# Optimization experiments

Hardware: AMD Instinct MI355X
Metric: run time of the kernel (lower is better)

## Reference

```python
import jax, jax.numpy as jnp
import numpy as np

T, B = 64, 64
E, H, V, L = 512, 1024, 32000, 2


def setup_inputs() -> dict:
    key = jax.random.key(0)
    ks = jax.random.split(key, 16)
    s = 0.05  # weight scale for numerical sanity
    return {
        "dec_input": jax.random.randint(ks[0], (T, B), 0, V),
        "enc_outputs": jax.random.normal(ks[1], (B, 48, H), jnp.float32),
        "h0": jax.random.normal(ks[2], (L, B, H), jnp.float32),
        "c0": jax.random.normal(ks[3], (L, B, H), jnp.float32),
        "emb_W": jax.random.normal(ks[4], (V, E), jnp.float32) * s,
        "W_ih0": jax.random.normal(ks[5], (4 * H, E), jnp.float32) * s,
        "W_hh0": jax.random.normal(ks[6], (4 * H, H), jnp.float32) * s,
        "b_ih0": jax.random.normal(ks[7], (4 * H,), jnp.float32) * s,
        "b_hh0": jax.random.normal(ks[8], (4 * H,), jnp.float32) * s,
        "W_ih1": jax.random.normal(ks[9], (4 * H, H), jnp.float32) * s,
        "W_hh1": jax.random.normal(ks[10], (4 * H, H), jnp.float32) * s,
        "b_ih1": jax.random.normal(ks[11], (4 * H,), jnp.float32) * s,
        "b_hh1": jax.random.normal(ks[12], (4 * H,), jnp.float32) * s,
        "W_out": jax.random.normal(ks[13], (V, H), jnp.float32) * s,
        "b_out": jax.random.normal(ks[14], (V,), jnp.float32) * s,
    }


def _lstm_cell(x, h, c, Wih, Whh, bih, bhh):
    # PyTorch LSTMCell gate order: i, f, g, o
    g = x @ Wih.T + bih + h @ Whh.T + bhh  # [B, 4H]
    i, f, gg, o = jnp.split(g, 4, axis=-1)
    c_n = jax.nn.sigmoid(f) * c + jax.nn.sigmoid(i) * jnp.tanh(gg)
    h_n = jax.nn.sigmoid(o) * jnp.tanh(c_n)
    return h_n, c_n


def reference(dec_input, enc_outputs, h0, c0, emb_W,
              W_ih0, W_hh0, b_ih0, b_hh0,
              W_ih1, W_hh1, b_ih1, b_hh1,
              W_out, b_out):
    emb = emb_W[dec_input]            # [T, B, E]
    xs = emb[:-1]                     # inputs for steps 0..T-2
    tgt = dec_input[1:]               # gather targets dec_input[t+1]

    def step(carry, inp):
        h, c, loss = carry            # h,c: [L, B, H]
        x, t = inp
        h0n, c0n = _lstm_cell(x, h[0], c[0], W_ih0, W_hh0, b_ih0, b_hh0)
        h1n, c1n = _lstm_cell(h0n, h[1], c[1], W_ih1, W_hh1, b_ih1, b_hh1)
        logits = h1n @ W_out.T + b_out              # [B, V]
        lp = jax.nn.log_softmax(logits, axis=-1)
        loss = loss - jnp.take_along_axis(lp, t[:, None], axis=1).sum()
        return (jnp.stack([h0n, h1n]), jnp.stack([c0n, c1n]), loss), None

    init = (h0, c0, jnp.zeros((), h0.dtype))
    (_, _, loss), _ = jax.lax.scan(step, init, (xs, tgt))
    return loss
```

## Files before the change

kernel.cpp:

```cpp
#include <hip/hip_runtime.h>
#include <math.h>

#define TSTEPS 63
#define BB 64
#define ED 512
#define HD 1024
#define VV 32000
#define GG 4096
#define NROWS 4032
#define MPAD 4096
#define NCH 500
#define PSTRIDE 262144

typedef __attribute__((ext_vector_type(8))) short short8;
typedef __attribute__((ext_vector_type(4))) float f32x4;

__device__ __forceinline__ float sigf(float x) { return 1.0f / (1.0f + __expf(-x)); }

__device__ __forceinline__ short f2bf(float f) {
  unsigned u = __float_as_uint(f);
  unsigned r = (u + 0x7FFFu + ((u >> 16) & 1u)) >> 16;
  return (short)r;
}

__global__ __launch_bounds__(256)
void init_state_k(const float* __restrict__ h0, const float* __restrict__ c0,
                  float* __restrict__ hs, float* __restrict__ cs) {
  int i = blockIdx.x * 256 + threadIdx.x;
  hs[i] = h0[i];
  cs[i] = c0[i];
}

__global__ __launch_bounds__(256)
void cvt_f2b_k(const float* __restrict__ src, short* __restrict__ dst) {
  int i = (blockIdx.x * 256 + threadIdx.x) * 4;
  float4 v = *(const float4*)(src + i);
  short4 o;
  o.x = f2bf(v.x); o.y = f2bf(v.y); o.z = f2bf(v.z); o.w = f2bf(v.w);
  *(short4*)(dst + i) = o;
}

__global__ __launch_bounds__(256)
void gather_emb_k(const int* __restrict__ dec, const float* __restrict__ emb,
                  short* __restrict__ XembB) {
  int idx = blockIdx.x * 256 + threadIdx.x;
  int r = idx >> 7, cc = (idx & 127) * 4;
  int src = dec[r];
  float4 v = *(const float4*)(emb + (size_t)src * ED + cc);
  short4 o;
  o.x = f2bf(v.x); o.y = f2bf(v.y); o.z = f2bf(v.z); o.w = f2bf(v.w);
  *(short4*)(XembB + (size_t)r * ED + cc) = o;
}

__global__ __launch_bounds__(256)
void pad_h1b_k(short* __restrict__ H1b) {
  int i = (blockIdx.x * 256 + threadIdx.x) * 4;
  short4 z; z.x = z.y = z.z = z.w = 0;
  *(short4*)(H1b + (size_t)NROWS * HD + i) = z;
}

__global__ void zero_out_k(float* __restrict__ out) {
  if (threadIdx.x == 0) out[0] = 0.f;
}

template<int NK>
__device__ __forceinline__ void mfma_loop(const short* __restrict__ Abase, int lda,
                                          const short* __restrict__ Bbase, int ldb,
                                          short* lds_a, short* lds_b,
                                          f32x4 acc[4][4]) {
  const int tid = threadIdx.x;
  const int l = tid & 63;
  const int w = tid >> 6;
  const int wm = w >> 1, wn = w & 1;
  const int p = tid & 7;
  const int rbase = tid >> 3;

  for (int kt = 0; kt < NK; kt++) {
#pragma unroll
    for (int it = 0; it < 4; it++) {
      int row = it * 32 + rbase;
      int ch = p ^ (row & 7);
      const short* ga = Abase + (size_t)row * lda + kt * 64 + ch * 8;
      const short* gb = Bbase + (size_t)row * ldb + kt * 64 + ch * 8;
      short* la = lds_a + it * 2048 + tid * 8;
      short* lb = lds_b + it * 2048 + tid * 8;
      __builtin_amdgcn_global_load_lds((const __attribute__((address_space(1))) void*)ga,
                                       (__attribute__((address_space(3))) void*)la, 16, 0, 0);
      __builtin_amdgcn_global_load_lds((const __attribute__((address_space(1))) void*)gb,
                                       (__attribute__((address_space(3))) void*)lb, 16, 0, 0);
    }
    asm volatile("s_waitcnt vmcnt(0)" ::: "memory");
    __syncthreads();

    short8 af[4][2], bf[4][2];
#pragma unroll
    for (int m = 0; m < 4; m++) {
#pragma unroll
      for (int ks = 0; ks < 2; ks++) {
        int ra = wm * 64 + m * 16 + (l & 15);
        int ca = (ks * 4 + (l >> 4)) ^ (ra & 7);
        af[m][ks] = *(const short8*)(lds_a + ra * 64 + ca * 8);
        int rb = wn * 64 + m * 16 + (l & 15);
        int cb = (ks * 4 + (l >> 4)) ^ (rb & 7);
        bf[m][ks] = *(const short8*)(lds_b + rb * 64 + cb * 8);
      }
    }
#pragma unroll
    for (int ks = 0; ks < 2; ks++)
#pragma unroll
      for (int m = 0; m < 4; m++)
#pragma unroll
        for (int n = 0; n < 4; n++)
          acc[m][n] = __builtin_amdgcn_mfma_f32_16x16x32_bf16(af[m][ks], bf[n][ks],
                                                              acc[m][n], 0, 0, 0);
    __syncthreads();
  }
}

__global__ __launch_bounds__(256)
void x0_mfma_k(const short* __restrict__ XembB, const short* __restrict__ Wih0B,
               const float* __restrict__ bih0, const float* __restrict__ bhh0,
               float* __restrict__ X0) {
  __shared__ short lds_a[128 * 64];
  __shared__ short lds_b[128 * 64];
  f32x4 acc[4][4];
#pragma unroll
  for (int m = 0; m < 4; m++)
#pragma unroll
    for (int n = 0; n < 4; n++)
#pragma unroll
      for (int q = 0; q < 4; q++) acc[m][n][q] = 0.f;

  mfma_loop<8>(XembB + (size_t)blockIdx.x * 128 * ED, ED,
               Wih0B + (size_t)blockIdx.y * 128 * ED, ED, lds_a, lds_b, acc);

  const int l = threadIdx.x & 63;
  const int w = threadIdx.x >> 6;
  const int wm = w >> 1, wn = w & 1;
#pragma unroll
  for (int m = 0; m < 4; m++)
#pragma unroll
    for (int r = 0; r < 4; r++) {
      int row = blockIdx.x * 128 + wm * 64 + m * 16 + (l >> 4) * 4 + r;
#pragma unroll
      for (int n = 0; n < 4; n++) {
        int col = blockIdx.y * 128 + wn * 64 + n * 16 + (l & 15);
        X0[(size_t)row * GG + col] = acc[m][n][r] + bih0[col] + bhh0[col];
      }
    }
}

__global__ __launch_bounds__(256)
void lse_mfma_k(const short* __restrict__ H1b, const short* __restrict__ WoutB,
                const float* __restrict__ bout, float* __restrict__ m_part,
                float* __restrict__ s_part) {
  __shared__ short lds_a[128 * 64];
  __shared__ short lds_b[128 * 64];
  f32x4 acc[4][4];
#pragma unroll
  for (int m = 0; m < 4; m++)
#pragma unroll
    for (int n = 0; n < 4; n++)
#pragma unroll
      for (int q = 0; q < 4; q++) acc[m][n][q] = 0.f;

  mfma_loop<16>(H1b + (size_t)blockIdx.x * 128 * HD, HD,
                WoutB + (size_t)blockIdx.y * 128 * HD, HD, lds_a, lds_b, acc);

  const int l = threadIdx.x & 63;
  const int w = threadIdx.x >> 6;
  const int wm = w >> 1, wn = w & 1;
  const int colbase = blockIdx.y * 128 + wn * 64 + (l & 15);
  float bo[4];
#pragma unroll
  for (int n = 0; n < 4; n++) bo[n] = bout[colbase + n * 16];
  const int ch = blockIdx.y * 2 + wn;

#pragma unroll
  for (int m = 0; m < 4; m++) {
#pragma unroll
    for (int r = 0; r < 4; r++) {
      float v0 = acc[m][0][r] + bo[0];
      float v1 = acc[m][1][r] + bo[1];
      float v2 = acc[m][2][r] + bo[2];
      float v3 = acc[m][3][r] + bo[3];
      float mx = fmaxf(fmaxf(v0, v1), fmaxf(v2, v3));
      float s = __expf(v0 - mx) + __expf(v1 - mx) + __expf(v2 - mx) + __expf(v3 - mx);
#pragma unroll
      for (int off = 1; off < 16; off <<= 1) {
        float mo = __shfl_xor(mx, off);
        float so = __shfl_xor(s, off);
        float nm = fmaxf(mx, mo);
        s = s * __expf(mx - nm) + so * __expf(mo - nm);
        mx = nm;
      }
      if ((l & 15) == 0) {
        int row = blockIdx.x * 128 + wm * 64 + m * 16 + (l >> 4) * 4 + r;
        m_part[(size_t)ch * MPAD + row] = mx;
        s_part[(size_t)ch * MPAD + row] = s;
      }
    }
  }
}

__global__ __launch_bounds__(256)
void rec_gemm_k(const float* __restrict__ A0, const float* __restrict__ W0,
                const float* __restrict__ A1, const float* __restrict__ W1,
                float* __restrict__ part) {
  __shared__ float As[16][68];
  __shared__ float Bs[16][68];
  int n0 = blockIdx.x * 64;
  int p  = blockIdx.y;
  const float* A = (p < 4) ? A0 : A1;
  const float* W = (p < 4) ? W0 : W1;
  int koff = (p & 3) * 256;
  int tid = threadIdx.x;
  int tx = tid & 15, ty = tid >> 4;
  int lm = tid >> 2, lk = (tid & 3) * 4;
  float acc[4][4] = {};
  for (int k0 = koff; k0 < koff + 256; k0 += 16) {
    float4 av = *(const float4*)(A + (size_t)lm * HD + k0 + lk);
    float4 bv = *(const float4*)(W + (size_t)(n0 + lm) * HD + k0 + lk);
    As[lk + 0][lm] = av.x; As[lk + 1][lm] = av.y; As[lk + 2][lm] = av.z; As[lk + 3][lm] = av.w;
    Bs[lk + 0][lm] = bv.x; Bs[lk + 1][lm] = bv.y; Bs[lk + 2][lm] = bv.z; Bs[lk + 3][lm] = bv.w;
    __syncthreads();
#pragma unroll
    for (int kk = 0; kk < 16; kk++) {
      float a4[4], b4[4];
      *(float4*)a4 = *(const float4*)&As[kk][ty * 4];
      *(float4*)b4 = *(const float4*)&Bs[kk][tx * 4];
#pragma unroll
      for (int i = 0; i < 4; i++)
#pragma unroll
        for (int j = 0; j < 4; j++) acc[i][j] += a4[i] * b4[j];
    }
    __syncthreads();
  }
  float* dst = part + (size_t)p * PSTRIDE;
#pragma unroll
  for (int i = 0; i < 4; i++)
#pragma unroll
    for (int j = 0; j < 4; j++)
      dst[(size_t)(ty * 4 + i) * GG + n0 + tx * 4 + j] = acc[i][j];
}

__global__ __launch_bounds__(256)
void cell0_k(const float* __restrict__ X0t, const float* __restrict__ part,
             float* __restrict__ h, float* __restrict__ c) {
  int idx = blockIdx.x * 256 + threadIdx.x;
  int b = idx >> 10, j = idx & (HD - 1);
  float g[4];
#pragma unroll
  for (int q = 0; q < 4; q++) {
    size_t o = (size_t)b * GG + q * HD + j;
    g[q] = X0t[o] + part[o] + part[o + PSTRIDE] + part[o + 2 * PSTRIDE] + part[o + 3 * PSTRIDE];
  }
  float cn = sigf(g[1]) * c[idx] + sigf(g[0]) * tanhf(g[2]);
  float hn = sigf(g[3]) * tanhf(cn);
  c[idx] = cn;
  h[idx] = hn;
}

__global__ __launch_bounds__(256)
void cell1_k(const float* __restrict__ part, const float* __restrict__ bih,
             const float* __restrict__ bhh, float* __restrict__ h,
             float* __restrict__ c, float* __restrict__ H1t,
             short* __restrict__ H1bt) {
  int idx = blockIdx.x * 256 + threadIdx.x;
  int b = idx >> 10, j = idx & (HD - 1);
  float g[4];
#pragma unroll
  for (int q = 0; q < 4; q++) {
    int gi = q * HD + j;
    size_t o = (size_t)b * GG + gi;
    float v = bih[gi] + bhh[gi];
#pragma unroll
    for (int p = 0; p < 8; p++) v += part[(size_t)p * PSTRIDE + o];
    g[q] = v;
  }
  float cn = sigf(g[1]) * c[idx] + sigf(g[0]) * tanhf(g[2]);
  float hn = sigf(g[3]) * tanhf(cn);
  c[idx] = cn;
  h[idx] = hn;
  H1t[idx] = hn;
  H1bt[idx] = f2bf(hn);
}

__global__ __launch_bounds__(256)
void tgt_logit_k(const float* __restrict__ H1, const float* __restrict__ Wout,
                 const float* __restrict__ bout, const int* __restrict__ dec,
                 float* __restrict__ tl) {
  int gw = (blockIdx.x * 256 + threadIdx.x) >> 6;
  int lane = threadIdx.x & 63;
  if (gw >= NROWS) return;
  int tgt = dec[gw + 64];
  const float* hrow = H1 + (size_t)gw * HD;
  const float* wrow = Wout + (size_t)tgt * HD;
  float s = 0.f;
#pragma unroll
  for (int q = 0; q < 16; q++) {
    int k = lane + q * 64;
    s += hrow[k] * wrow[k];
  }
#pragma unroll
  for (int off = 32; off > 0; off >>= 1) s += __shfl_down(s, off);
  if (lane == 0) tl[gw] = s + bout[tgt];
}

__global__ __launch_bounds__(256)
void row_lse_k(const float* __restrict__ m_part, const float* __restrict__ s_part,
               const float* __restrict__ tl, float* __restrict__ out) {
  int row = blockIdx.x * 256 + threadIdx.x;
  float loss = 0.f;
  if (row < NROWS) {
    float M = -INFINITY, S = 0.f;
    for (int ch = 0; ch < NCH; ch++) {
      float m = m_part[(size_t)ch * MPAD + row];
      float s = s_part[(size_t)ch * MPAD + row];
      float nm = fmaxf(M, m);
      S = S * __expf(M - nm) + s * __expf(m - nm);
      M = nm;
    }
    loss = M + logf(S) - tl[row];
  }
  __shared__ float red[256];
  red[threadIdx.x] = loss;
  __syncthreads();
  for (int s = 128; s > 0; s >>= 1) {
    if (threadIdx.x < s) red[threadIdx.x] += red[threadIdx.x + s];
    __syncthreads();
  }
  if (threadIdx.x == 0) atomicAdd(out, red[0]);
}

extern "C" void kernel_launch(void* const* d_in, const int* in_sizes, int n_in,
                              void* d_out, int out_size, void* d_ws, size_t ws_size,
                              hipStream_t stream) {
  const int*   dec  = (const int*)  d_in[0];
  const float* h0   = (const float*)d_in[2];
  const float* c0   = (const float*)d_in[3];
  const float* emb  = (const float*)d_in[4];
  const float* Wih0 = (const float*)d_in[5];
  const float* Whh0 = (const float*)d_in[6];
  const float* bih0 = (const float*)d_in[7];
  const float* bhh0 = (const float*)d_in[8];
  const float* Wih1 = (const float*)d_in[9];
  const float* Whh1 = (const float*)d_in[10];
  const float* bih1 = (const float*)d_in[11];
  const float* bhh1 = (const float*)d_in[12];
  const float* Wout = (const float*)d_in[13];
  const float* bout = (const float*)d_in[14];
  float* out = (float*)d_out;

  float* ws = (float*)d_ws;
  float* X0     = ws;
  float* H1     = X0 + (size_t)MPAD * GG;
  float* hs     = H1 + (size_t)NROWS * HD;
  float* cs     = hs + 2 * BB * HD;
  float* part   = cs + 2 * BB * HD;
  float* m_part = part + 8 * (size_t)BB * GG;
  float* s_part = m_part + (size_t)NCH * MPAD;
  float* tl     = s_part + (size_t)NCH * MPAD;
  short* H1b    = (short*)(tl + MPAD);
  short* WoutB  = H1b + (size_t)MPAD * HD;
  short* Wih0B  = WoutB + (size_t)VV * HD;
  short* XembB  = Wih0B + (size_t)GG * ED;

  float* hs0 = hs, * hs1 = hs + BB * HD;
  float* cs0 = cs, * cs1 = cs + BB * HD;

  init_state_k<<<(2 * BB * HD) / 256, 256, 0, stream>>>(h0, c0, hs, cs);
  cvt_f2b_k<<<(VV * HD) / 1024, 256, 0, stream>>>(Wout, WoutB);
  cvt_f2b_k<<<(GG * ED) / 1024, 256, 0, stream>>>(Wih0, Wih0B);
  gather_emb_k<<<(MPAD * ED / 4) / 256, 256, 0, stream>>>(dec, emb, XembB);
  pad_h1b_k<<<64, 256, 0, stream>>>(H1b);
  zero_out_k<<<1, 64, 0, stream>>>(out);
  x0_mfma_k<<<dim3(MPAD / 128, GG / 128), 256, 0, stream>>>(XembB, Wih0B, bih0, bhh0, X0);

  for (int t = 0; t < TSTEPS; t++) {
    rec_gemm_k<<<dim3(64, 4), 256, 0, stream>>>(hs0, Whh0, hs0, Whh0, part);
    cell0_k<<<256, 256, 0, stream>>>(X0 + (size_t)t * BB * GG, part, hs0, cs0);
    rec_gemm_k<<<dim3(64, 8), 256, 0, stream>>>(hs0, Wih1, hs1, Whh1, part);
    cell1_k<<<256, 256, 0, stream>>>(part, bih1, bhh1, hs1, cs1,
                                     H1 + (size_t)t * BB * HD, H1b + (size_t)t * BB * HD);
  }

  tgt_logit_k<<<(NROWS * 64 + 255) / 256, 256, 0, stream>>>(H1, Wout, bout, dec, tl);
  lse_mfma_k<<<dim3(MPAD / 128, VV / 128), 256, 0, stream>>>(H1b, WoutB, bout, m_part, s_part);
  row_lse_k<<<MPAD / 256, 256, 0, stream>>>(m_part, s_part, tl, out);
}
```

Baseline: 3.319 ms.

## Fuse LSTM recurrence into one persistent cooperative kernel with bf16 MFMA

Replaces the 252 per-step launches of fp32 split-K GEMMs and cell kernels with a single cooperative kernel of 96 blocks. Within each grid-synced phase, layer 0 for step t runs alongside layer 1 for step t-1, so the two layers overlap as a wavefront. The recurrent weights are converted to bf16 and the GEMMs use MFMA with double-buffered LDS staging, and the gate nonlinearities are fused in so the split-K partial buffers are no longer needed. The trade-off is reduced precision in the recurrent state (h stored as bf16), and each phase now pays a grid-wide barrier while only 96 blocks do the work.

```diff
diff --git a/kernel.cpp b/kernel.cpp
--- a/kernel.cpp
+++ b/kernel.cpp
@@ -1,4 +1,5 @@
 #include <hip/hip_runtime.h>
+#include <hip/hip_cooperative_groups.h>
 #include <math.h>
 
 #define TSTEPS 63
@@ -10,7 +11,7 @@
 #define NROWS 4032
 #define MPAD 4096
 #define NCH 500
-#define PSTRIDE 262144
+#define HSLOT 65536
 
 typedef __attribute__((ext_vector_type(8))) short short8;
 typedef __attribute__((ext_vector_type(4))) float f32x4;
@@ -22,14 +23,13 @@
   unsigned r = (u + 0x7FFFu + ((u >> 16) & 1u)) >> 16;
   return (short)r;
 }
-
-__global__ __launch_bounds__(256)
-void init_state_k(const float* __restrict__ h0, const float* __restrict__ c0,
-                  float* __restrict__ hs, float* __restrict__ cs) {
-  int i = blockIdx.x * 256 + threadIdx.x;
-  hs[i] = h0[i];
-  cs[i] = c0[i];
-}
+__device__ __forceinline__ float bf2f(short h) {
+  return __uint_as_float(((unsigned)(unsigned short)h) << 16);
+}
+
+#define GLOAD_LDS(g, l) \
+  __builtin_amdgcn_global_load_lds((const __attribute__((address_space(1))) void*)(g), \
+                                   (__attribute__((address_space(3))) void*)(l), 16, 0, 0)
 
 __global__ __launch_bounds__(256)
 void cvt_f2b_k(const float* __restrict__ src, short* __restrict__ dst) {
@@ -53,10 +53,28 @@
 }
 
 __global__ __launch_bounds__(256)
-void pad_h1b_k(short* __restrict__ H1b) {
+void init_state2_k(const float* __restrict__ h0, const float* __restrict__ c0,
+                   short* __restrict__ h0buf, short* __restrict__ H1b,
+                   float* __restrict__ c0s, float* __restrict__ c1s) {
+  int i = blockIdx.x * 256 + threadIdx.x;
+  h0buf[HSLOT + i] = f2bf(h0[i]);
+  H1b[i] = f2bf(h0[BB * HD + i]);
+  c0s[i] = c0[i];
+  c1s[i] = c0[BB * HD + i];
+}
+
+__global__ __launch_bounds__(256)
+void bias_sum_k(const float* __restrict__ a, const float* __restrict__ b,
+                float* __restrict__ s) {
+  int i = blockIdx.x * 256 + threadIdx.x;
+  s[i] = a[i] + b[i];
+}
+
+__global__ __launch_bounds__(256)
+void pad_h1b_k(short* __restrict__ dst) {
   int i = (blockIdx.x * 256 + threadIdx.x) * 4;
   short4 z; z.x = z.y = z.z = z.w = 0;
-  *(short4*)(H1b + (size_t)NROWS * HD + i) = z;
+  *(short4*)(dst + i) = z;
 }
 
 __global__ void zero_out_k(float* __restrict__ out) {
@@ -84,10 +102,8 @@
       const short* gb = Bbase + (size_t)row * ldb + kt * 64 + ch * 8;
       short* la = lds_a + it * 2048 + tid * 8;
       short* lb = lds_b + it * 2048 + tid * 8;
-      __builtin_amdgcn_global_load_lds((const __attribute__((address_space(1))) void*)ga,
-                                       (__attribute__((address_space(3))) void*)la, 16, 0, 0);
-      __builtin_amdgcn_global_load_lds((const __attribute__((address_space(1))) void*)gb,
-                                       (__attribute__((address_space(3))) void*)lb, 16, 0, 0);
+      GLOAD_LDS(ga, la);
+      GLOAD_LDS(gb, lb);
     }
     asm volatile("s_waitcnt vmcnt(0)" ::: "memory");
     __syncthreads();
@@ -150,8 +166,190 @@
     }
 }
 
-__global__ __launch_bounds__(256)
-void lse_mfma_k(const short* __restrict__ H1b, const short* __restrict__ WoutB,
+__global__ __launch_bounds__(256, 1)
+void recurrence_k(const float* __restrict__ X0, const float* __restrict__ bsum1,
+                  const short* __restrict__ Wh0b, const short* __restrict__ Wi1b,
+                  const short* __restrict__ Wh1b, short* __restrict__ h0buf,
+                  short* __restrict__ H1b, float* __restrict__ c0s,
+                  float* __restrict__ c1s) {
+  cooperative_groups::grid_group grid = cooperative_groups::this_grid();
+  __shared__ short lA[2][4096];
+  __shared__ short lB[2][8192];
+  const int tid = threadIdx.x;
+  const int l   = tid & 63;
+  const int w   = tid >> 6;
+  const int p8  = tid & 7;
+  const int r32 = tid >> 3;
+  const int lj  = l & 15;
+  const int lh  = l >> 4;
+  const bool isA = (blockIdx.x < 32);
+  const int g = isA ? (int)blockIdx.x : (int)blockIdx.x - 32;
+
+  for (int ph = 0; ph < 64; ph++) {
+    if (isA && ph < TSTEPS) {
+      const int t = ph;
+      const int jb = g * 32;
+      const short* Ab = h0buf + ((t + 1) & 1) * HSLOT;
+      f32x4 acc[8];
+#pragma unroll
+      for (int f = 0; f < 8; f++)
+#pragma unroll
+        for (int q = 0; q < 4; q++) acc[f][q] = 0.f;
+
+      auto stage0 = [&](int kt, int buf) {
+#pragma unroll
+        for (int it = 0; it < 2; it++) {
+          int row = it * 32 + r32;
+          int ch = p8 ^ (row & 7);
+          GLOAD_LDS(Ab + (size_t)row * HD + kt * 64 + ch * 8,
+                    &lA[buf][it * 2048 + tid * 8]);
+        }
+#pragma unroll
+        for (int it = 0; it < 4; it++) {
+          int row = it * 32 + r32;
+          int grow = (row >> 5) * HD + jb + (row & 31);
+          int ch = p8 ^ (row & 7);
+          GLOAD_LDS(Wh0b + (size_t)grow * HD + kt * 64 + ch * 8,
+                    &lB[buf][it * 2048 + tid * 8]);
+        }
+      };
+
+      stage0(0, 0);
+      __syncthreads();
+      for (int kt = 0; kt < 16; kt++) {
+        int cur = kt & 1;
+        if (kt < 15) stage0(kt + 1, cur ^ 1);
+        int ra = w * 16 + lj;
+        short8 af[2];
+#pragma unroll
+        for (int ks = 0; ks < 2; ks++) {
+          int ca = (ks * 4 + lh) ^ (ra & 7);
+          af[ks] = *(const short8*)&lA[cur][ra * 64 + ca * 8];
+        }
+#pragma unroll
+        for (int f = 0; f < 8; f++) {
+          int rb = f * 16 + lj;
+#pragma unroll
+          for (int ks = 0; ks < 2; ks++) {
+            int cb = (ks * 4 + lh) ^ (rb & 7);
+            short8 bfr = *(const short8*)&lB[cur][rb * 64 + cb * 8];
+            acc[f] = __builtin_amdgcn_mfma_f32_16x16x32_bf16(af[ks], bfr, acc[f], 0, 0, 0);
+          }
+        }
+        __syncthreads();
+      }
+      const float* X0t = X0 + (size_t)t * BB * GG;
+      short* hdst = h0buf + (t & 1) * HSLOT;
+#pragma unroll
+      for (int jj = 0; jj < 2; jj++) {
+        int j = jb + jj * 16 + lj;
+#pragma unroll
+        for (int r = 0; r < 4; r++) {
+          int b = w * 16 + lh * 4 + r;
+          float gi = acc[0 + jj][r] + X0t[(size_t)b * GG + j];
+          float gf = acc[2 + jj][r] + X0t[(size_t)b * GG + HD + j];
+          float gg = acc[4 + jj][r] + X0t[(size_t)b * GG + 2 * HD + j];
+          float go = acc[6 + jj][r] + X0t[(size_t)b * GG + 3 * HD + j];
+          float cp = c0s[b * HD + j];
+          float cn = sigf(gf) * cp + sigf(gi) * tanhf(gg);
+          float hn = sigf(go) * tanhf(cn);
+          c0s[b * HD + j] = cn;
+          hdst[b * HD + j] = f2bf(hn);
+        }
+      }
+    } else if (!isA && ph >= 1) {
+      const int t = ph - 1;
+      const int jb = g * 16;
+      f32x4 acc[4];
+#pragma unroll
+      for (int f = 0; f < 4; f++)
+#pragma unroll
+        for (int q = 0; q < 4; q++) acc[f][q] = 0.f;
+
+      auto stage1 = [&](int u, int buf) {
+        int seg = u >> 4, kt = u & 15;
+        const short* Ab = seg ? (H1b + (size_t)t * HSLOT) : (h0buf + (t & 1) * HSLOT);
+        const short* Wb = seg ? Wh1b : Wi1b;
+#pragma unroll
+        for (int it = 0; it < 2; it++) {
+          int row = it * 32 + r32;
+          int ch = p8 ^ (row & 7);
+          GLOAD_LDS(Ab + (size_t)row * HD + kt * 64 + ch * 8,
+                    &lA[buf][it * 2048 + tid * 8]);
+          int grow = (row >> 4) * HD + jb + (row & 15);
+          GLOAD_LDS(Wb + (size_t)grow * HD + kt * 64 + ch * 8,
+                    &lB[buf][it * 2048 + tid * 8]);
+        }
+      };
+
+      stage1(0, 0);
+      __syncthreads();
+      for (int u = 0; u < 32; u++) {
+        int cur = u & 1;
+        if (u < 31) stage1(u + 1, cur ^ 1);
+        int ra = w * 16 + lj;
+        short8 af[2];
+#pragma unroll
+        for (int ks = 0; ks < 2; ks++) {
+          int ca = (ks * 4 + lh) ^ (ra & 7);
+          af[ks] = *(const short8*)&lA[cur][ra * 64 + ca * 8];
+        }
+#pragma unroll
+        for (int f = 0; f < 4; f++) {
+          int rb = f * 16 + lj;
+#pragma unroll
+          for (int ks = 0; ks < 2; ks++) {
+            int cb = (ks * 4 + lh) ^ (rb & 7);
+            short8 bfr = *(const short8*)&lB[cur][rb * 64 + cb * 8];
+            acc[f] = __builtin_amdgcn_mfma_f32_16x16x32_bf16(af[ks], bfr, acc[f], 0, 0, 0);
+          }
+        }
+        __syncthreads();
+      }
+      int j = jb + lj;
+      short* hdst = H1b + (size_t)(t + 1) * HSLOT;
+#pragma unroll
+      for (int r = 0; r < 4; r++) {
+        int b = w * 16 + lh * 4 + r;
+        float gi = acc[0][r] + bsum1[j];
+        float gf = acc[1][r] + bsum1[HD + j];
+        float gg = acc[2][r] + bsum1[2 * HD + j];
+        float go = acc[3][r] + bsum1[3 * HD + j];
+        float cp = c1s[b * HD + j];
+        float cn = sigf(gf) * cp + sigf(gi) * tanhf(gg);
+        float hn = sigf(go) * tanhf(cn);
+        c1s[b * HD + j] = cn;
+        hdst[b * HD + j] = f2bf(hn);
+      }
+    }
+    __threadfence();
+    grid.sync();
+  }
+}
+
+__global__ __launch_bounds__(256)
+void tgt_logit_k(const short* __restrict__ H1log, const float* __restrict__ Wout,
+                 const float* __restrict__ bout, const int* __restrict__ dec,
+                 float* __restrict__ tl) {
+  int gw = (blockIdx.x * 256 + threadIdx.x) >> 6;
+  int lane = threadIdx.x & 63;
+  if (gw >= NROWS) return;
+  int tgt = dec[gw + 64];
+  const short* hrow = H1log + (size_t)gw * HD;
+  const float* wrow = Wout + (size_t)tgt * HD;
+  float s = 0.f;
+#pragma unroll
+  for (int q = 0; q < 16; q++) {
+    int k = lane + q * 64;
+    s += bf2f(hrow[k]) * wrow[k];
+  }
+#pragma unroll
+  for (int off = 32; off > 0; off >>= 1) s += __shfl_down(s, off);
+  if (lane == 0) tl[gw] = s + bout[tgt];
+}
+
+__global__ __launch_bounds__(256)
+void lse_mfma_k(const short* __restrict__ H1log, const short* __restrict__ WoutB,
                 const float* __restrict__ bout, float* __restrict__ m_part,
                 float* __restrict__ s_part) {
   __shared__ short lds_a[128 * 64];
@@ -164,7 +362,7 @@
 #pragma unroll
       for (int q = 0; q < 4; q++) acc[m][n][q] = 0.f;
 
-  mfma_loop<16>(H1b + (size_t)blockIdx.x * 128 * HD, HD,
+  mfma_loop<16>(H1log + (size_t)blockIdx.x * 128 * HD, HD,
                 WoutB + (size_t)blockIdx.y * 128 * HD, HD, lds_a, lds_b, acc);
 
   const int l = threadIdx.x & 63;
@@ -201,110 +399,6 @@
       }
     }
   }
-}
-
-__global__ __launch_bounds__(256)
-void rec_gemm_k(const float* __restrict__ A0, const float* __restrict__ W0,
-                const float* __restrict__ A1, const float* __restrict__ W1,
-                float* __restrict__ part) {
-  __shared__ float As[16][68];
-  __shared__ float Bs[16][68];
-  int n0 = blockIdx.x * 64;
-  int p  = blockIdx.y;
-  const float* A = (p < 4) ? A0 : A1;
-  const float* W = (p < 4) ? W0 : W1;
-  int koff = (p & 3) * 256;
-  int tid = threadIdx.x;
-  int tx = tid & 15, ty = tid >> 4;
-  int lm = tid >> 2, lk = (tid & 3) * 4;
-  float acc[4][4] = {};
-  for (int k0 = koff; k0 < koff + 256; k0 += 16) {
-    float4 av = *(const float4*)(A + (size_t)lm * HD + k0 + lk);
-    float4 bv = *(const float4*)(W + (size_t)(n0 + lm) * HD + k0 + lk);
-    As[lk + 0][lm] = av.x; As[lk + 1][lm] = av.y; As[lk + 2][lm] = av.z; As[lk + 3][lm] = av.w;
-    Bs[lk + 0][lm] = bv.x; Bs[lk + 1][lm] = bv.y; Bs[lk + 2][lm] = bv.z; Bs[lk + 3][lm] = bv.w;
-    __syncthreads();
-#pragma unroll
-    for (int kk = 0; kk < 16; kk++) {
-      float a4[4], b4[4];
-      *(float4*)a4 = *(const float4*)&As[kk][ty * 4];
-      *(float4*)b4 = *(const float4*)&Bs[kk][tx * 4];
-#pragma unroll
-      for (int i = 0; i < 4; i++)
-#pragma unroll
-        for (int j = 0; j < 4; j++) acc[i][j] += a4[i] * b4[j];
-    }
-    __syncthreads();
-  }
-  float* dst = part + (size_t)p * PSTRIDE;
-#pragma unroll
-  for (int i = 0; i < 4; i++)
-#pragma unroll
-    for (int j = 0; j < 4; j++)
-      dst[(size_t)(ty * 4 + i) * GG + n0 + tx * 4 + j] = acc[i][j];
-}
-
-__global__ __launch_bounds__(256)
-void cell0_k(const float* __restrict__ X0t, const float* __restrict__ part,
-             float* __restrict__ h, float* __restrict__ c) {
-  int idx = blockIdx.x * 256 + threadIdx.x;
-  int b = idx >> 10, j = idx & (HD - 1);
-  float g[4];
-#pragma unroll
-  for (int q = 0; q < 4; q++) {
-    size_t o = (size_t)b * GG + q * HD + j;
-    g[q] = X0t[o] + part[o] + part[o + PSTRIDE] + part[o + 2 * PSTRIDE] + part[o + 3 * PSTRIDE];
-  }
-  float cn = sigf(g[1]) * c[idx] + sigf(g[0]) * tanhf(g[2]);
-  float hn = sigf(g[3]) * tanhf(cn);
-  c[idx] = cn;
-  h[idx] = hn;
-}
-
-__global__ __launch_bounds__(256)
-void cell1_k(const float* __restrict__ part, const float* __restrict__ bih,
-             const float* __restrict__ bhh, float* __restrict__ h,
-             float* __restrict__ c, float* __restrict__ H1t,
-             short* __restrict__ H1bt) {
-  int idx = blockIdx.x * 256 + threadIdx.x;
-  int b = idx >> 10, j = idx & (HD - 1);
-  float g[4];
-#pragma unroll
-  for (int q = 0; q < 4; q++) {
-    int gi = q * HD + j;
-    size_t o = (size_t)b * GG + gi;
-    float v = bih[gi] + bhh[gi];
-#pragma unroll
-    for (int p = 0; p < 8; p++) v += part[(size_t)p * PSTRIDE + o];
-    g[q] = v;
-  }
-  float cn = sigf(g[1]) * c[idx] + sigf(g[0]) * tanhf(g[2]);
-  float hn = sigf(g[3]) * tanhf(cn);
-  c[idx] = cn;
-  h[idx] = hn;
-  H1t[idx] = hn;
-  H1bt[idx] = f2bf(hn);
-}
-
-__global__ __launch_bounds__(256)
-void tgt_logit_k(const float* __restrict__ H1, const float* __restrict__ Wout,
-                 const float* __restrict__ bout, const int* __restrict__ dec,
-                 float* __restrict__ tl) {
-  int gw = (blockIdx.x * 256 + threadIdx.x) >> 6;
-  int lane = threadIdx.x & 63;
-  if (gw >= NROWS) return;
-  int tgt = dec[gw + 64];
-  const float* hrow = H1 + (size_t)gw * HD;
-  const float* wrow = Wout + (size_t)tgt * HD;
-  float s = 0.f;
-#pragma unroll
-  for (int q = 0; q < 16; q++) {
-    int k = lane + q * 64;
-    s += hrow[k] * wrow[k];
-  }
-#pragma unroll
-  for (int off = 32; off > 0; off >>= 1) s += __shfl_down(s, off);
-  if (lane == 0) tl[gw] = s + bout[tgt];
 }
 
 __global__ __launch_bounds__(256)
@@ -354,38 +448,38 @@
 
   float* ws = (float*)d_ws;
   float* X0     = ws;
-  float* H1     = X0 + (size_t)MPAD * GG;
-  float* hs     = H1 + (size_t)NROWS * HD;
-  float* cs     = hs + 2 * BB * HD;
-  float* part   = cs + 2 * BB * HD;
-  float* m_part = part + 8 * (size_t)BB * GG;
+  float* m_part = X0 + (size_t)MPAD * GG;
   float* s_part = m_part + (size_t)NCH * MPAD;
   float* tl     = s_part + (size_t)NCH * MPAD;
-  short* H1b    = (short*)(tl + MPAD);
-  short* WoutB  = H1b + (size_t)MPAD * HD;
+  float* c0s    = tl + MPAD;
+  float* c1s    = c0s + BB * HD;
+  float* bsum1  = c1s + BB * HD;
+  short* H1b    = (short*)(bsum1 + GG);
+  short* WoutB  = H1b + HSLOT + (size_t)MPAD * HD;
   short* Wih0B  = WoutB + (size_t)VV * HD;
   short* XembB  = Wih0B + (size_t)GG * ED;
-
-  float* hs0 = hs, * hs1 = hs + BB * HD;
-  float* cs0 = cs, * cs1 = cs + BB * HD;
-
-  init_state_k<<<(2 * BB * HD) / 256, 256, 0, stream>>>(h0, c0, hs, cs);
+  short* Wh0b   = XembB + (size_t)MPAD * ED;
+  short* Wi1b   = Wh0b + (size_t)GG * HD;
+  short* Wh1b   = Wi1b + (size_t)GG * HD;
+  short* h0buf  = Wh1b + (size_t)GG * HD;
+  short* H1log  = H1b + HSLOT;
+
   cvt_f2b_k<<<(VV * HD) / 1024, 256, 0, stream>>>(Wout, WoutB);
   cvt_f2b_k<<<(GG * ED) / 1024, 256, 0, stream>>>(Wih0, Wih0B);
+  cvt_f2b_k<<<(GG * HD) / 1024, 256, 0, stream>>>(Whh0, Wh0b);
+  cvt_f2b_k<<<(GG * HD) / 1024, 256, 0, stream>>>(Wih1, Wi1b);
+  cvt_f2b_k<<<(GG * HD) / 1024, 256, 0, stream>>>(Whh1, Wh1b);
   gather_emb_k<<<(MPAD * ED / 4) / 256, 256, 0, stream>>>(dec, emb, XembB);
-  pad_h1b_k<<<64, 256, 0, stream>>>(H1b);
+  init_state2_k<<<256, 256, 0, stream>>>(h0, c0, h0buf, H1b, c0s, c1s);
+  bias_sum_k<<<16, 256, 0, stream>>>(bih1, bhh1, bsum1);
+  pad_h1b_k<<<64, 256, 0, stream>>>(H1log + (size_t)NROWS * HD);
   zero_out_k<<<1, 64, 0, stream>>>(out);
   x0_mfma_k<<<dim3(MPAD / 128, GG / 128), 256, 0, stream>>>(XembB, Wih0B, bih0, bhh0, X0);
 
-  for (int t = 0; t < TSTEPS; t++) {
-    rec_gemm_k<<<dim3(64, 4), 256, 0, stream>>>(hs0, Whh0, hs0, Whh0, part);
-    cell0_k<<<256, 256, 0, stream>>>(X0 + (size_t)t * BB * GG, part, hs0, cs0);
-    rec_gemm_k<<<dim3(64, 8), 256, 0, stream>>>(hs0, Wih1, hs1, Whh1, part);
-    cell1_k<<<256, 256, 0, stream>>>(part, bih1, bhh1, hs1, cs1,
-                                     H1 + (size_t)t * BB * HD, H1b + (size_t)t * BB * HD);
-  }
-
-  tgt_logit_k<<<(NROWS * 64 + 255) / 256, 256, 0, stream>>>(H1, Wout, bout, dec, tl);
-  lse_mfma_k<<<dim3(MPAD / 128, VV / 128), 256, 0, stream>>>(H1b, WoutB, bout, m_part, s_part);
+  void* args[] = {&X0, &bsum1, &Wh0b, &Wi1b, &Wh1b, &h0buf, &H1b, &c0s, &c1s};
+  hipLaunchCooperativeKernel((void*)recurrence_k, dim3(96), dim3(256), args, 0, stream);
+
+  tgt_logit_k<<<(NROWS * 64 + 255) / 256, 256, 0, stream>>>(H1log, Wout, bout, dec, tl);
+  lse_mfma_k<<<dim3(MPAD / 128, VV / 128), 256, 0, stream>>>(H1log, WoutB, bout, m_part, s_part);
   row_lse_k<<<MPAD / 256, 256, 0, stream>>>(m_part, s_part, tl, out);
 }
```

After: 3.543 ms. +6.7%, slower.
